# Kernel optimization log

Hardware: AMD Instinct MI355X
Metric: run time of the kernel (lower is better)

## Reference

```python
import jax, jax.numpy as jnp
import numpy as np

N = 250000
E = 4000000
IN_F, HID, OUT = 18, 16, 1


def setup_inputs() -> dict:
    key = jax.random.key(0)
    ks = jax.random.split(key, 7)
    x = jax.random.normal(ks[0], (N, IN_F), dtype=jnp.float32)
    edge_index = jax.random.randint(ks[1], (2, E), 0, N, dtype=jnp.int64)
    # GCNConv params (PyG uses Glorot for weight, zeros for bias)
    W1 = jax.random.normal(ks[2], (IN_F, HID), dtype=jnp.float32) * (1.0 / np.sqrt(IN_F))
    b1 = jnp.zeros((HID,), dtype=jnp.float32)
    W2 = jax.random.normal(ks[3], (HID, OUT), dtype=jnp.float32) * (1.0 / np.sqrt(HID))
    b2 = jnp.zeros((OUT,), dtype=jnp.float32)
    return {"x": x, "edge_index": edge_index, "W1": W1, "b1": b1, "W2": W2, "b2": b2}


def _gcn_conv(x, W, b, src, dst, norm, n_nodes):
    # linear transform then degree-normalized scatter-add (PyG GCNConv)
    h = x @ W                                  # [N, F_out]
    msg = h[src] * norm[:, None]               # gather + per-edge scale
    out = jax.ops.segment_sum(msg, dst, num_segments=n_nodes)
    return out + b


def reference(x, edge_index, W1, b1, W2, b2):
    # add self-loops (GCNConv default add_self_loops=True)
    loops = jnp.arange(N, dtype=edge_index.dtype)
    src = jnp.concatenate([edge_index[0], loops])
    dst = jnp.concatenate([edge_index[1], loops])
    # symmetric normalization: deg computed at destination over self-looped graph
    deg = jax.ops.segment_sum(jnp.ones_like(dst, dtype=x.dtype), dst, num_segments=N)
    dis = jnp.where(deg > 0, jax.lax.rsqrt(deg), 0.0)
    norm = dis[src] * dis[dst]                 # [E+N]
    h = _gcn_conv(x, W1, b1, src, dst, norm, N)
    h = jax.nn.relu(h)
    # dropout is identity in eval mode (F.dropout(training=self.training))
    out = _gcn_conv(h, W2, b2, src, dst, norm, N)
    return out
```

## Files before the change

### kernel.cpp

```cpp
#include <hip/hip_runtime.h>
#include <hip/hip_fp16.h>


#define NB_BITS 8
#define BN (1 << NB_BITS)
#define SB_BITS 9
#define SBN (1 << SB_BITS)
#define NSB 512
#define BIN_TPB 512
#define BIN_CHUNK 8192
#define AGG_TPB 512

__global__ void bhist_kernel(const int* __restrict__ dst, int* __restrict__ bcnt, int E) {
    __shared__ int cnt[NSB];
    int t = threadIdx.x;
    cnt[t] = 0;
    __syncthreads();
    int base = blockIdx.x * BIN_CHUNK;
    int end = min(base + BIN_CHUNK, E);
#pragma unroll 4
    for (int e = base + t; e < end; e += BIN_TPB)
        atomicAdd(&cnt[dst[e] >> SB_BITS], 1);
    __syncthreads();
    if (cnt[t] > 0) atomicAdd(&bcnt[t], cnt[t]);
}

__global__ void bscan_kernel(const int* __restrict__ bcnt, int* __restrict__ bstart,
                             int* __restrict__ cursor) {
    __shared__ int s[NSB];
    int t = threadIdx.x;
    int v = bcnt[t];
    s[t] = v;
    __syncthreads();
    for (int off = 1; off < NSB; off <<= 1) {
        int add = (t >= off) ? s[t - off] : 0;
        __syncthreads();
        s[t] += add;
        __syncthreads();
    }
    int excl = s[t] - v;
    bstart[t] = excl;
    cursor[t] = excl;
    if (t == NSB - 1) bstart[NSB] = s[t];
}

__global__ void bplace_kernel(const int* __restrict__ src, const int* __restrict__ dst,
                              int* __restrict__ cursor, int* __restrict__ pairs, int E) {
    __shared__ int cnt[NSB];
    __shared__ int lstart[NSB];
    __shared__ int lcur[NSB];
    __shared__ int gbase[NSB];
    __shared__ int lbuf[BIN_CHUNK];
    __shared__ unsigned short lbin[BIN_CHUNK];
    int t = threadIdx.x;
    int base = blockIdx.x * BIN_CHUNK;
    int end = min(base + BIN_CHUNK, E);
    cnt[t] = 0;
    __syncthreads();
#pragma unroll 4
    for (int e = base + t; e < end; e += BIN_TPB)
        atomicAdd(&cnt[dst[e] >> SB_BITS], 1);
    __syncthreads();
    int v = cnt[t];
    lstart[t] = v;
    __syncthreads();
    for (int off = 1; off < NSB; off <<= 1) {
        int add = (t >= off) ? lstart[t - off] : 0;
        __syncthreads();
        lstart[t] += add;
        __syncthreads();
    }
    int excl = lstart[t] - v;
    lstart[t] = excl;
    lcur[t] = excl;
    gbase[t] = (v > 0) ? atomicAdd(&cursor[t], v) : 0;
    __syncthreads();
#pragma unroll 2
    for (int e = base + t; e < end; e += BIN_TPB) {
        int d = dst[e], s = src[e];
        int b = d >> SB_BITS;
        int pos = atomicAdd(&lcur[b], 1);
        lbuf[pos] = (s << SB_BITS) | (d & (SBN - 1));
        lbin[pos] = (unsigned short)b;
    }
    __syncthreads();
    int n = end - base;
#pragma unroll 4
    for (int i = t; i < n; i += BIN_TPB) {
        int b = lbin[i];
        pairs[gbase[b] + (i - lstart[b])] = lbuf[i];
    }
}

__global__ void csr_kernel(const int* __restrict__ pairs, const int* __restrict__ bstart,
                           int* __restrict__ rowp, int* __restrict__ csr_src,
                           float* __restrict__ dis, int N) {
    __shared__ int cnt[SBN];
    __shared__ int tmp[SBN];
    int b = blockIdx.x, t = threadIdx.x;
    int s0 = bstart[b], s1 = bstart[b + 1];
    cnt[t] = 0;
    __syncthreads();
#pragma unroll 4
    for (int e = s0 + t; e < s1; e += SBN)
        atomicAdd(&cnt[pairs[e] & (SBN - 1)], 1);
    __syncthreads();
    int v = cnt[t];
    tmp[t] = v;
    __syncthreads();
    for (int off = 1; off < SBN; off <<= 1) {
        int add = (t >= off) ? tmp[t - off] : 0;
        __syncthreads();
        tmp[t] += add;
        __syncthreads();
    }
    int nbase = b << SB_BITS;
    int start = s0 + tmp[t] - v;
    rowp[nbase + t] = start;
    int n = nbase + t;
    if (n < N) dis[n] = rsqrtf((float)v + 1.0f);
    cnt[t] = start;
    if (t == 0) rowp[nbase + SBN] = s1;
    __syncthreads();
#pragma unroll 4
    for (int e = s0 + t; e < s1; e += SBN) {
        int pv = pairs[e];
        int pos = atomicAdd(&cnt[pv & (SBN - 1)], 1);
        csr_src[pos] = pv >> SB_BITS;
    }
}

__global__ void h1_kernel(const float* __restrict__ x, const float* __restrict__ W1,
                          const float* __restrict__ dis, __half* __restrict__ hs1h, int N) {
    __shared__ float w[18 * 16];
    for (int i = threadIdx.x; i < 18 * 16; i += blockDim.x) w[i] = W1[i];
    __syncthreads();
    int n = blockIdx.x * blockDim.x + threadIdx.x;
    if (n >= N) return;
    const float2* x2 = (const float2*)(x + (size_t)n * 18);
    float xv[18];
#pragma unroll
    for (int k = 0; k < 9; k++) {
        float2 v = x2[k];
        xv[2 * k] = v.x;
        xv[2 * k + 1] = v.y;
    }
    float d = dis[n];
    float acc[16];
#pragma unroll
    for (int f = 0; f < 16; f++) acc[f] = 0.0f;
#pragma unroll
    for (int k = 0; k < 18; k++) {
        float xk = xv[k];
#pragma unroll
        for (int f = 0; f < 16; f++) acc[f] = fmaf(xk, w[k * 16 + f], acc[f]);
    }
    unsigned int u[8];
#pragma unroll
    for (int q = 0; q < 8; q++) {
        unsigned int lo = __half_as_ushort(__float2half_rn(acc[2 * q] * d));
        unsigned int hi = __half_as_ushort(__float2half_rn(acc[2 * q + 1] * d));
        u[q] = lo | (hi << 16);
    }
    uint4* outp = (uint4*)(hs1h + (size_t)n * 16);
    outp[0] = make_uint4(u[0], u[1], u[2], u[3]);
    outp[1] = make_uint4(u[4], u[5], u[6], u[7]);
}

__global__ void agg1_kernel(const int* __restrict__ csr_src, const int* __restrict__ rowp,
                            const __half* __restrict__ hs1h, const float* __restrict__ dis,
                            const float* __restrict__ b1, const float* __restrict__ W2,
                            float* __restrict__ hs2, int N) {
    int b = blockIdx.x, t = threadIdx.x;
    int f = t & 15;
    int g = t >> 4;
    float bbf = b1[f], wwf = W2[f];
    int nbase = b << NB_BITS;
    for (int nl = g; nl < BN; nl += AGG_TPB / 16) {
        int n = nbase + nl;
        if (n >= N) continue;
        int r0 = rowp[n], r1 = rowp[n + 1];
        float a = 0.f;
#pragma unroll 4
        for (int r = r0; r < r1; ++r) {
            int s = csr_src[r];
            a += __half2float(hs1h[(size_t)s * 16 + f]);
        }
        float d = dis[n];
        float self = __half2float(hs1h[(size_t)n * 16 + f]);
        float p = fmaxf(d * (a + self) + bbf, 0.f) * wwf;
        p += __shfl_xor(p, 1);
        p += __shfl_xor(p, 2);
        p += __shfl_xor(p, 4);
        p += __shfl_xor(p, 8);
        if (f == 0) hs2[n] = p * d;
    }
}

__global__ void agg2_kernel(const int* __restrict__ csr_src, const int* __restrict__ rowp,
                            const float* __restrict__ hs2, const float* __restrict__ dis,
                            const float* __restrict__ b2, float* __restrict__ out, int N) {
    int b = blockIdx.x, t = threadIdx.x;
    int l = t & 15;
    int g = t >> 4;
    int nbase = b << NB_BITS;
    float bb = b2[0];
    for (int nl = g; nl < BN; nl += AGG_TPB / 16) {
        int n = nbase + nl;
        if (n >= N) continue;
        int r0 = rowp[n], r1 = rowp[n + 1];
        float a = 0.f;
        for (int r = r0 + l; r < r1; r += 16) a += hs2[csr_src[r]];
        a += __shfl_xor(a, 1);
        a += __shfl_xor(a, 2);
        a += __shfl_xor(a, 4);
        a += __shfl_xor(a, 8);
        if (l == 0) out[n] = dis[n] * (a + hs2[n]) + bb;
    }
}

extern "C" void kernel_launch(void* const* d_in, const int* in_sizes, int n_in,
                              void* d_out, int out_size, void* d_ws, size_t ws_size,
                              hipStream_t stream) {
    const float* x = (const float*)d_in[0];
    const int* edge_index = (const int*)d_in[1];
    const float* W1 = (const float*)d_in[2];
    const float* b1 = (const float*)d_in[3];
    const float* W2 = (const float*)d_in[4];
    const float* b2 = (const float*)d_in[5];
    float* out = (float*)d_out;

    const int N = in_sizes[0] / 18;
    const int E = in_sizes[1] / 2;
    const int* src = edge_index;
    const int* dst = edge_index + E;
    const int NABUCKET = (N + BN - 1) / BN;
    const int NSBUCKET = (N + SBN - 1) / SBN;

    int* ws = (int*)d_ws;
    int* pairs = ws;
    int* csr_src = pairs + (size_t)E;
    __half* hs1h = (__half*)(csr_src + (size_t)E);
    float* hs2 = (float*)((int*)(csr_src + (size_t)E) + 8 * (size_t)N);
    float* dis = hs2 + N;
    int* rowp = (int*)(dis + N);
    int* bstart = rowp + (size_t)NSBUCKET * SBN + 1;
    int* cursor = bstart + NSB + 1;
    int* bcnt = cursor + NSB;

    hipMemsetAsync(bcnt, 0, NSB * sizeof(int), stream);

    int binBlocks = (E + BIN_CHUNK - 1) / BIN_CHUNK;
    int nBlocksN = (N + 255) / 256;

    bhist_kernel<<<binBlocks, BIN_TPB, 0, stream>>>(dst, bcnt, E);
    bscan_kernel<<<1, NSB, 0, stream>>>(bcnt, bstart, cursor);
    bplace_kernel<<<binBlocks, BIN_TPB, 0, stream>>>(src, dst, cursor, pairs, E);
    csr_kernel<<<NSBUCKET, SBN, 0, stream>>>(pairs, bstart, rowp, csr_src, dis, N);
    h1_kernel<<<nBlocksN, 256, 0, stream>>>(x, W1, dis, hs1h, N);
    agg1_kernel<<<NABUCKET, AGG_TPB, 0, stream>>>(csr_src, rowp, hs1h, dis, b1, W2, hs2, N);
    agg2_kernel<<<NABUCKET, AGG_TPB, 0, stream>>>(csr_src, rowp, hs2, dis, b2, out, N);
}
```

Measured before the change: 254.1 us.

## Split layer-1 features into two 8-wide halves aggregated in separate passes

The 16-feature fp16 hidden array is split into two planar arrays of 8 features each, and the layer-1 aggregation runs as two kernels, each gathering 16-byte rows instead of 32-byte rows. The first pass writes a partial ReLU·W2 dot product and the second adds its half and the degree scale. The aim is to shrink each pass's random-gather working set (4 MB per half) so it fits better in cache. Nontemporal loads are added for the CSR index streams so they do not evict the feature data. The cost is reading the CSR structure twice and one extra launch.

```diff
diff --git a/kernel.cpp b/kernel.cpp
--- a/kernel.cpp
+++ b/kernel.cpp
@@ -131,7 +131,8 @@
 }
 
 __global__ void h1_kernel(const float* __restrict__ x, const float* __restrict__ W1,
-                          const float* __restrict__ dis, __half* __restrict__ hs1h, int N) {
+                          const float* __restrict__ dis, __half* __restrict__ hs1a,
+                          __half* __restrict__ hs1b, int N) {
     __shared__ float w[18 * 16];
     for (int i = threadIdx.x; i < 18 * 16; i += blockDim.x) w[i] = W1[i];
     __syncthreads();
@@ -162,38 +163,68 @@
         unsigned int hi = __half_as_ushort(__float2half_rn(acc[2 * q + 1] * d));
         u[q] = lo | (hi << 16);
     }
-    uint4* outp = (uint4*)(hs1h + (size_t)n * 16);
-    outp[0] = make_uint4(u[0], u[1], u[2], u[3]);
-    outp[1] = make_uint4(u[4], u[5], u[6], u[7]);
-}
-
-__global__ void agg1_kernel(const int* __restrict__ csr_src, const int* __restrict__ rowp,
-                            const __half* __restrict__ hs1h, const float* __restrict__ dis,
-                            const float* __restrict__ b1, const float* __restrict__ W2,
-                            float* __restrict__ hs2, int N) {
+    *(uint4*)(hs1a + (size_t)n * 8) = make_uint4(u[0], u[1], u[2], u[3]);
+    *(uint4*)(hs1b + (size_t)n * 8) = make_uint4(u[4], u[5], u[6], u[7]);
+}
+
+__global__ void agg1a_kernel(const int* __restrict__ csr_src, const int* __restrict__ rowp,
+                             const __half* __restrict__ hs1a, const float* __restrict__ dis,
+                             const float* __restrict__ b1, const float* __restrict__ W2,
+                             float* __restrict__ partial, int N) {
     int b = blockIdx.x, t = threadIdx.x;
-    int f = t & 15;
-    int g = t >> 4;
+    int f = t & 7;
+    int g = t >> 3;
     float bbf = b1[f], wwf = W2[f];
     int nbase = b << NB_BITS;
-    for (int nl = g; nl < BN; nl += AGG_TPB / 16) {
+    for (int nl = g; nl < BN; nl += AGG_TPB / 8) {
         int n = nbase + nl;
         if (n >= N) continue;
-        int r0 = rowp[n], r1 = rowp[n + 1];
+        int r0 = __builtin_nontemporal_load(rowp + n);
+        int r1 = __builtin_nontemporal_load(rowp + n + 1);
         float a = 0.f;
 #pragma unroll 4
         for (int r = r0; r < r1; ++r) {
-            int s = csr_src[r];
-            a += __half2float(hs1h[(size_t)s * 16 + f]);
+            int s = __builtin_nontemporal_load(csr_src + r);
+            a += __half2float(hs1a[(size_t)s * 8 + f]);
         }
         float d = dis[n];
-        float self = __half2float(hs1h[(size_t)n * 16 + f]);
+        float self = __half2float(hs1a[(size_t)n * 8 + f]);
         float p = fmaxf(d * (a + self) + bbf, 0.f) * wwf;
         p += __shfl_xor(p, 1);
         p += __shfl_xor(p, 2);
         p += __shfl_xor(p, 4);
-        p += __shfl_xor(p, 8);
-        if (f == 0) hs2[n] = p * d;
+        if (f == 0) partial[n] = p;
+    }
+}
+
+__global__ void agg1b_kernel(const int* __restrict__ csr_src, const int* __restrict__ rowp,
+                             const __half* __restrict__ hs1b, const float* __restrict__ dis,
+                             const float* __restrict__ b1, const float* __restrict__ W2,
+                             const float* __restrict__ partial, float* __restrict__ hs2,
+                             int N) {
+    int b = blockIdx.x, t = threadIdx.x;
+    int f = t & 7;
+    int g = t >> 3;
+    float bbf = b1[8 + f], wwf = W2[8 + f];
+    int nbase = b << NB_BITS;
+    for (int nl = g; nl < BN; nl += AGG_TPB / 8) {
+        int n = nbase + nl;
+        if (n >= N) continue;
+        int r0 = __builtin_nontemporal_load(rowp + n);
+        int r1 = __builtin_nontemporal_load(rowp + n + 1);
+        float a = 0.f;
+#pragma unroll 4
+        for (int r = r0; r < r1; ++r) {
+            int s = __builtin_nontemporal_load(csr_src + r);
+            a += __half2float(hs1b[(size_t)s * 8 + f]);
+        }
+        float d = dis[n];
+        float self = __half2float(hs1b[(size_t)n * 8 + f]);
+        float p = fmaxf(d * (a + self) + bbf, 0.f) * wwf;
+        p += __shfl_xor(p, 1);
+        p += __shfl_xor(p, 2);
+        p += __shfl_xor(p, 4);
+        if (f == 0) hs2[n] = (partial[n] + p) * d;
     }
 }
 
@@ -210,7 +241,8 @@
         if (n >= N) continue;
         int r0 = rowp[n], r1 = rowp[n + 1];
         float a = 0.f;
-        for (int r = r0 + l; r < r1; r += 16) a += hs2[csr_src[r]];
+        for (int r = r0 + l; r < r1; r += 16)
+            a += hs2[__builtin_nontemporal_load(csr_src + r)];
         a += __shfl_xor(a, 1);
         a += __shfl_xor(a, 2);
         a += __shfl_xor(a, 4);
@@ -240,8 +272,10 @@
     int* ws = (int*)d_ws;
     int* pairs = ws;
     int* csr_src = pairs + (size_t)E;
-    __half* hs1h = (__half*)(csr_src + (size_t)E);
-    float* hs2 = (float*)((int*)(csr_src + (size_t)E) + 8 * (size_t)N);
+    __half* hs1a = (__half*)(csr_src + (size_t)E);
+    __half* hs1b = (__half*)((int*)(csr_src + (size_t)E) + 4 * (size_t)N);
+    float* partial = (float*)((int*)(csr_src + (size_t)E) + 8 * (size_t)N);
+    float* hs2 = partial + N;
     float* dis = hs2 + N;
     int* rowp = (int*)(dis + N);
     int* bstart = rowp + (size_t)NSBUCKET * SBN + 1;
@@ -257,7 +291,10 @@
     bscan_kernel<<<1, NSB, 0, stream>>>(bcnt, bstart, cursor);
     bplace_kernel<<<binBlocks, BIN_TPB, 0, stream>>>(src, dst, cursor, pairs, E);
     csr_kernel<<<NSBUCKET, SBN, 0, stream>>>(pairs, bstart, rowp, csr_src, dis, N);
-    h1_kernel<<<nBlocksN, 256, 0, stream>>>(x, W1, dis, hs1h, N);
-    agg1_kernel<<<NABUCKET, AGG_TPB, 0, stream>>>(csr_src, rowp, hs1h, dis, b1, W2, hs2, N);
+    h1_kernel<<<nBlocksN, 256, 0, stream>>>(x, W1, dis, hs1a, hs1b, N);
+    agg1a_kernel<<<NABUCKET, AGG_TPB, 0, stream>>>(csr_src, rowp, hs1a, dis, b1, W2,
+                                                   partial, N);
+    agg1b_kernel<<<NABUCKET, AGG_TPB, 0, stream>>>(csr_src, rowp, hs1b, dis, b1, W2,
+                                                   partial, hs2, N);
     agg2_kernel<<<NABUCKET, AGG_TPB, 0, stream>>>(csr_src, rowp, hs2, dis, b2, out, N);
 }
```

Result: slower. 297.4 us (+17.1%).
